# Kernel tuning notes

Measured on AMD Instinct MI355X. Metric: run time of the kernel, lower is better.

## Reference

```python
import jax, jax.numpy as jnp
import numpy as np

N_HEADS = 16
EPS = 1e-6  # WanSelfAttention passes eps=1e-6 to WanRMSNorm
ROPE_MAX = 1024


def _rmsnorm(v, g):
    # WanRMSNorm: normalize in fp32 over the full `dim`, then scale by weight
    v32 = v.astype(jnp.float32)
    n = v32 * jax.lax.rsqrt(jnp.mean(v32 * v32, axis=-1, keepdims=True) + EPS)
    return n * g


def _rope(x, f, h, w, fc, fs):
    # x: [b, s, n, d] with s == f*h*w. Complex rope: (a+bi) * (cos + i sin)
    b, s, n, d = x.shape
    c = d // 2
    c1 = c - 2 * (c // 3)
    c2 = c // 3

    def build(t):  # t: [ROPE_MAX, c] -> [1, s, 1, c]
        tf, th, tw = t[:, :c1], t[:, c1:c1 + c2], t[:, c1 + c2:]
        pf = jnp.broadcast_to(tf[:f, None, None, :], (f, h, w, c1))
        ph = jnp.broadcast_to(th[None, :h, None, :], (f, h, w, c2))
        pw = jnp.broadcast_to(tw[None, None, :w, :], (f, h, w, c2))
        return jnp.concatenate([pf, ph, pw], axis=-1).reshape(1, f * h * w, 1, c)

    cosv, sinv = build(fc), build(fs)
    xr = x.astype(jnp.float32).reshape(b, s, n, c, 2)
    a, bi = xr[..., 0], xr[..., 1]
    out_r = a * cosv - bi * sinv
    out_i = a * sinv + bi * cosv
    return jnp.stack([out_r, out_i], axis=-1).reshape(b, s, n, d)


def setup_inputs() -> dict:
    key = jax.random.key(0)
    ks = jax.random.split(key, 12)
    b, s, dim = 1, 2048, 2048
    n, d = N_HEADS, 2048 // N_HEADS  # d = 128, c = 64
    f, h, w = 2, 32, 32              # f*h*w == s
    c = d // 2
    c1 = c - 2 * (c // 3)
    c2 = c // 3

    # Realistic rope tables per band (cos/sin of pos * inv_freq)
    pos = np.arange(ROPE_MAX, dtype=np.float64)[:, None]
    ang = []
    for cx in (c1, c2, c2):
        inv = 1.0 / (10000.0 ** (np.arange(cx, dtype=np.float64) / cx))
        ang.append(pos * inv[None, :])
    ang = np.concatenate(ang, axis=1)
    freqs_cos = jnp.asarray(np.cos(ang), dtype=jnp.float32)
    freqs_sin = jnp.asarray(np.sin(ang), dtype=jnp.float32)

    scale = 1.0 / np.sqrt(dim)
    inp = {
        "x": jax.random.normal(ks[0], (b, s, dim), dtype=jnp.float32),
        "freqs_cos": freqs_cos,
        "freqs_sin": freqs_sin,
        "Wq": jax.random.normal(ks[1], (dim, dim), dtype=jnp.float32) * scale,
        "bq": jnp.zeros((dim,), dtype=jnp.float32),
        "Wk": jax.random.normal(ks[2], (dim, dim), dtype=jnp.float32) * scale,
        "bk": jnp.zeros((dim,), dtype=jnp.float32),
        "Wv": jax.random.normal(ks[3], (dim, dim), dtype=jnp.float32) * scale,
        "bv": jnp.zeros((dim,), dtype=jnp.float32),
        "Wo": jax.random.normal(ks[4], (dim, dim), dtype=jnp.float32) * scale,
        "bo": jnp.zeros((dim,), dtype=jnp.float32),
        "gq": jnp.ones((dim,), dtype=jnp.float32),
        "gk": jnp.ones((dim,), dtype=jnp.float32),
        "seq_lens": jnp.array([s], dtype=jnp.int32),
        "f": f,
        "h": h,
        "w": w,
    }
    return inp


def reference(x, freqs_cos, freqs_sin, Wq, bq, Wk, bk, Wv, bv, Wo, bo, gq, gk,
              seq_lens, f, h, w):
    b, s, dim = x.shape
    n = N_HEADS
    d = dim // n

    q = _rmsnorm(x @ Wq.T + bq, gq).reshape(b, s, n, d)
    k = _rmsnorm(x @ Wk.T + bk, gk).reshape(b, s, n, d)
    v = (x @ Wv.T + bv).reshape(b, s, n, d)

    q = _rope(q, f, h, w, freqs_cos, freqs_sin)
    k = _rope(k, f, h, w, freqs_cos, freqs_sin)

    scale = np.float32(1.0 / np.sqrt(d))
    scores = jnp.einsum('bqnd,bknd->bnqk', q, k) * scale  # [b,n,s,s]
    key_mask = jnp.arange(s)[None, :] < seq_lens[:, None]  # [b,s] (k_lens)
    scores = jnp.where(key_mask[:, None, None, :], scores, -jnp.inf)
    probs = jax.nn.softmax(scores, axis=-1)
    out = jnp.einsum('bnqk,bknd->bqnd', probs, v).reshape(b, s, dim)
    return out @ Wo.T + bo
```

## Files before the change

kernel.cpp:

```cpp
#include <hip/hip_runtime.h>
#include <cstdint>
#include <cmath>

typedef unsigned int uint;
typedef unsigned short ushort;
typedef __bf16 bf16_t;
typedef bf16_t bf16x8 __attribute__((ext_vector_type(8)));
typedef float f32x4 __attribute__((ext_vector_type(4)));
typedef float f32x16 __attribute__((ext_vector_type(16)));

#define LOG2E 1.44269504088896340736f

__device__ __forceinline__ ushort f2bf(float f) {
  uint x = __float_as_uint(f);
  x += 0x7fffu + ((x >> 16) & 1u);
  return (ushort)(x >> 16);
}
__device__ __forceinline__ uint pack2(float lo, float hi) {
  return (uint)f2bf(lo) | ((uint)f2bf(hi) << 16);
}
__device__ __forceinline__ uint cvt_pk_bf16(float lo, float hi) {
  uint r;
  asm("v_cvt_pk_bf16_f32 %0, %1, %2" : "=v"(r) : "v"(lo), "v"(hi));
  return r;
}

__device__ __forceinline__ void gload_lds16(const void* gsrc, void* ldsdst) {
  typedef const __attribute__((address_space(1))) unsigned int* gp_t;
  typedef __attribute__((address_space(3))) unsigned int* lp_t;
  __builtin_amdgcn_global_load_lds((gp_t)(uintptr_t)gsrc,
                                   (lp_t)(unsigned int)(uintptr_t)ldsdst,
                                   16, 0, 0);
}

__global__ __launch_bounds__(256) void cvt5(const float* __restrict__ x,
                                            const float* __restrict__ wq,
                                            const float* __restrict__ wk,
                                            const float* __restrict__ wv,
                                            const float* __restrict__ wo,
                                            ushort* __restrict__ xb,
                                            ushort* __restrict__ wqkv,
                                            ushort* __restrict__ wob,
                                            int nx8, int nw8) {
  const int y = blockIdx.y;
  const float* src;
  ushort* dst;
  int n8;
  if (y == 0)      { src = x;  dst = xb;  n8 = nx8; }
  else if (y == 4) { src = wo; dst = wob; n8 = nw8; }
  else {
    src = (y == 1) ? wq : (y == 2) ? wk : wv;
    dst = wqkv + (size_t)(y - 1) * nw8 * 8;
    n8 = nw8;
  }
  int i = blockIdx.x * blockDim.x + threadIdx.x;
  if (i >= n8) return;
  const float4* s4 = (const float4*)src;
  float4 a = s4[i * 2], b = s4[i * 2 + 1];
  uint4 o;
  o.x = pack2(a.x, a.y); o.y = pack2(a.z, a.w);
  o.z = pack2(b.x, b.y); o.w = pack2(b.z, b.w);
  ((uint4*)dst)[i] = o;
}

__global__ __launch_bounds__(512) void gemm_qkv192(const ushort* __restrict__ A,
                                                   const ushort* __restrict__ B,
                                                   const float* __restrict__ bq,
                                                   const float* __restrict__ bk,
                                                   const float* __restrict__ bv,
                                                   float* __restrict__ qpre,
                                                   float* __restrict__ kpre,
                                                   ushort* __restrict__ Vt,
                                                   int K, int S_) {
  __shared__ __align__(16) unsigned char ldsA[65536];
  __shared__ __align__(16) unsigned char ldsB[49152];
  const int t = threadIdx.x, l = t & 63;
  const int w = t >> 6;
  const int g = l >> 4, c = l & 15;
  const int wr = w >> 2, wc = w & 3;
  const int tm = blockIdx.y * 256, tn = blockIdx.x * 192;

  const int srow = t >> 3;
  const int schunk = (t & 7) ^ (srow & 7);
  const ushort* Ag = A + (size_t)(tm + srow) * K + schunk * 8;
  const ushort* Bg = B + (size_t)(tn + srow) * K + schunk * 8;
  const size_t rK64 = (size_t)64 * K;

#define STG_A(kt, u) gload_lds16(Ag + (size_t)(u) * rK64 + ((kt) << 6),   \
    ldsA + ((kt)&1) * 32768 + (u) * 8192 + t * 16)
#define STG_B(kt, u) gload_lds16(Bg + (size_t)(u) * rK64 + ((kt) << 6),   \
    ldsB + ((kt)&1) * 24576 + (u) * 8192 + t * 16)

  f32x4 acc[8][3] = {};
  bf16x8 af[2][2], bfr[3][2];
  const int cr = c * 128;
  const int sw0 = ((0 * 4 + g) ^ (c & 7)) << 4;
  const int sw1 = ((1 * 4 + g) ^ (c & 7)) << 4;

#define RDA(d, q) do {                                                               \
    _Pragma("unroll") for (int mm = 0; mm < 2; ++mm) {                               \
      const unsigned char* p_ = ldsA + (d)*32768 + (wr*128 + (q)*32 + mm*16)*128 + cr; \
      af[mm][0] = *(const bf16x8*)(p_ + sw0);                                        \
      af[mm][1] = *(const bf16x8*)(p_ + sw1); }                                      \
  } while (0)
#define RDB(d) do {                                                                 \
    _Pragma("unroll") for (int nn = 0; nn < 3; ++nn) {                              \
      const unsigned char* p_ = ldsB + (d)*24576 + (wc*48 + nn*16)*128 + cr;        \
      bfr[nn][0] = *(const bf16x8*)(p_ + sw0);                                      \
      bfr[nn][1] = *(const bf16x8*)(p_ + sw1); }                                    \
  } while (0)
#define MM(q) do {                                                                  \
    __builtin_amdgcn_s_setprio(1);                                                  \
    _Pragma("unroll") for (int mm = 0; mm < 2; ++mm)                                \
    _Pragma("unroll") for (int nn = 0; nn < 3; ++nn) {                              \
      acc[(q)*2+mm][nn] = __builtin_amdgcn_mfma_f32_16x16x32_bf16(                  \
          af[mm][0], bfr[nn][0], acc[(q)*2+mm][nn], 0, 0, 0);                       \
      acc[(q)*2+mm][nn] = __builtin_amdgcn_mfma_f32_16x16x32_bf16(                  \
          af[mm][1], bfr[nn][1], acc[(q)*2+mm][nn], 0, 0, 0); }                     \
    __builtin_amdgcn_s_setprio(0);                                                  \
  } while (0)
#define BAR() __builtin_amdgcn_s_barrier()

  STG_B(0, 0); STG_B(0, 1); STG_B(0, 2);
  STG_A(0, 0); STG_A(0, 1); STG_A(0, 2); STG_A(0, 3);
  STG_B(1, 0); STG_B(1, 1); STG_B(1, 2);
  STG_A(1, 0); STG_A(1, 1); STG_A(1, 2);
  asm volatile("s_waitcnt vmcnt(6)" ::: "memory");
  BAR();

  const int NITER = K >> 7;
  for (int i = 0; i < NITER; ++i) {
    const int k1 = 2 * i + 1, k2 = 2 * i + 2, k3 = 2 * i + 3;
    const bool st = (i + 1 < NITER);
    RDA(0, 0); RDB(0);
    STG_A(k1, 3);
    MM(0); BAR();
    RDA(0, 1);
    if (st) { STG_B(k2, 0); STG_B(k2, 1); }
    MM(1); BAR();
    RDA(0, 2);
    if (st) { STG_B(k2, 2); STG_A(k2, 0); }
    MM(2); BAR();
    RDA(0, 3);
    if (st) { STG_A(k2, 1); STG_A(k2, 2); }
    MM(3);
    if (st) asm volatile("s_waitcnt vmcnt(6)" ::: "memory");
    else    asm volatile("s_waitcnt vmcnt(0)" ::: "memory");
    BAR();
    RDA(1, 0); RDB(1);
    if (st) STG_A(k2, 3);
    MM(0); BAR();
    RDA(1, 1);
    if (st) { STG_B(k3, 0); STG_B(k3, 1); }
    MM(1); BAR();
    RDA(1, 2);
    if (st) { STG_B(k3, 2); STG_A(k3, 0); }
    MM(2); BAR();
    RDA(1, 3);
    if (st) { STG_A(k3, 1); STG_A(k3, 2); }
    MM(3);
    if (st) asm volatile("s_waitcnt vmcnt(6)" ::: "memory");
    else    asm volatile("s_waitcnt vmcnt(0)" ::: "memory");
    BAR();
  }

#undef STG_A
#undef STG_B
#undef RDA
#undef RDB
#undef MM
#undef BAR

#pragma unroll
  for (int n = 0; n < 3; ++n) {
    int col = tn + wc * 48 + n * 16 + c;
    int sel = col >> 11;
    if (sel < 2) {
      float* outp = sel ? kpre : qpre;
      const float* bias = sel ? bk : bq;
      int col2 = col & 2047;
      float bvv = bias[col2];
#pragma unroll
      for (int m = 0; m < 8; ++m) {
        int row0 = tm + wr * 128 + m * 16 + g * 4;
#pragma unroll
        for (int i = 0; i < 4; ++i)
          outp[(size_t)(row0 + i) * 2048 + col2] = acc[m][n][i] + bvv;
      }
    } else {
      int colv = col - 4096;
      float bvv = bv[colv];
#pragma unroll
      for (int m = 0; m < 8; ++m) {
        int row0 = tm + wr * 128 + m * 16 + g * 4;
        uint2 o;
        o.x = pack2(acc[m][n][0] + bvv, acc[m][n][1] + bvv);
        o.y = pack2(acc[m][n][2] + bvv, acc[m][n][3] + bvv);
        *(uint2*)(Vt + (size_t)colv * S_ + row0) = o;
      }
    }
  }
}

__global__ __launch_bounds__(512) void gemm_wo8p(const ushort* __restrict__ A,
                                                 const ushort* __restrict__ B,
                                                 const float* __restrict__ bo,
                                                 float* __restrict__ out, int K) {
  __shared__ __align__(16) unsigned char ldsA[32768];
  __shared__ __align__(16) unsigned char ldsB[32768];
  const int t = threadIdx.x, l = t & 63;
  const int w = t >> 6;
  const int g = l >> 4, c = l & 15;
  const int wr = w >> 2, wc = w & 3;
  const int tm = blockIdx.y * 128, tn = blockIdx.x * 128;

  const int srow = t >> 3;
  const int schunk = (t & 7) ^ (srow & 7);
  const ushort* Ag = A + (size_t)(tm + srow) * K + schunk * 8;
  const ushort* Bg = B + (size_t)(tn + srow) * K + schunk * 8;
  const size_t rK64 = (size_t)64 * K;

#define WSTG_A(kt, u) gload_lds16(Ag + (size_t)(u) * rK64 + ((kt) << 6),   \
    ldsA + ((kt)&1) * 16384 + (u) * 8192 + t * 16)
#define WSTG_B(kt, u) gload_lds16(Bg + (size_t)(u) * rK64 + ((kt) << 6),   \
    ldsB + ((kt)&1) * 16384 + (u) * 8192 + t * 16)

  f32x4 acc[4][2] = {};
  bf16x8 af[2][2], bfr[2][2];
  const int cr = c * 128;
  const int sw0 = ((0 * 4 + g) ^ (c & 7)) << 4;
  const int sw1 = ((1 * 4 + g) ^ (c & 7)) << 4;

#define WRDA(d, hf) do {                                                             \
    _Pragma("unroll") for (int mm = 0; mm < 2; ++mm) {                               \
      const unsigned char* p_ = ldsA + (d)*16384 + (wr*64 + ((hf)*2+mm)*16)*128 + cr; \
      af[mm][0] = *(const bf16x8*)(p_ + sw0);                                        \
      af[mm][1] = *(const bf16x8*)(p_ + sw1); }                                      \
  } while (0)
#define WRDB(d) do {                                                                \
    _Pragma("unroll") for (int nn = 0; nn < 2; ++nn) {                              \
      const unsigned char* p_ = ldsB + (d)*16384 + (wc*32 + nn*16)*128 + cr;        \
      bfr[nn][0] = *(const bf16x8*)(p_ + sw0);                                      \
      bfr[nn][1] = *(const bf16x8*)(p_ + sw1); }                                    \
  } while (0)
#define WMM(hf) do {                                                                \
    __builtin_amdgcn_s_setprio(1);                                                  \
    _Pragma("unroll") for (int mm = 0; mm < 2; ++mm)                                \
    _Pragma("unroll") for (int nn = 0; nn < 2; ++nn) {                              \
      acc[(hf)*2+mm][nn] = __builtin_amdgcn_mfma_f32_16x16x32_bf16(                 \
          af[mm][0], bfr[nn][0], acc[(hf)*2+mm][nn], 0, 0, 0);                      \
      acc[(hf)*2+mm][nn] = __builtin_amdgcn_mfma_f32_16x16x32_bf16(                 \
          af[mm][1], bfr[nn][1], acc[(hf)*2+mm][nn], 0, 0, 0); }                    \
    __builtin_amdgcn_s_setprio(0);                                                  \
  } while (0)
#define WBAR() __builtin_amdgcn_s_barrier()

  WSTG_B(0, 0); WSTG_B(0, 1); WSTG_A(0, 0); WSTG_A(0, 1);
  WSTG_B(1, 0); WSTG_B(1, 1);
  asm volatile("s_waitcnt vmcnt(2)" ::: "memory");
  WBAR();

  const int NITER = K >> 7;
  for (int i = 0; i < NITER; ++i) {
    const int k1 = 2 * i + 1, k2 = 2 * i + 2, k3 = 2 * i + 3;
    const bool st = (i + 1 < NITER);
    WRDA(0, 0); WRDB(0);
    WSTG_A(k1, 0); WSTG_A(k1, 1);
    WMM(0); WBAR();
    WRDA(0, 1);
    if (st) { WSTG_B(k2, 0); WSTG_B(k2, 1); }
    WMM(1);
    if (st) asm volatile("s_waitcnt vmcnt(2)" ::: "memory");
    else    asm volatile("s_waitcnt vmcnt(0)" ::: "memory");
    WBAR();
    WRDA(1, 0); WRDB(1);
    if (st) { WSTG_A(k2, 0); WSTG_A(k2, 1); }
    WMM(0); WBAR();
    WRDA(1, 1);
    if (st) { WSTG_B(k3, 0); WSTG_B(k3, 1); }
    WMM(1);
    if (st) asm volatile("s_waitcnt vmcnt(2)" ::: "memory");
    else    asm volatile("s_waitcnt vmcnt(0)" ::: "memory");
    WBAR();
  }

#undef WSTG_A
#undef WSTG_B
#undef WRDA
#undef WRDB
#undef WMM
#undef WBAR

#pragma unroll
  for (int n = 0; n < 2; ++n) {
    int col = tn + wc * 32 + n * 16 + c;
    float bvv = bo[col];
#pragma unroll
    for (int m = 0; m < 4; ++m) {
      int row0 = tm + wr * 64 + m * 16 + g * 4;
#pragma unroll
      for (int i = 0; i < 4; ++i)
        out[(size_t)(row0 + i) * 2048 + col] = acc[m][n][i] + bvv;
    }
  }
}

__global__ __launch_bounds__(256) void fuse_rms_rope(const float* __restrict__ qpre,
                                                     const float* __restrict__ kpre,
                                                     const float* __restrict__ gq,
                                                     const float* __restrict__ gk,
                                                     const float* __restrict__ fc,
                                                     const float* __restrict__ fs,
                                                     const int* __restrict__ pH,
                                                     const int* __restrict__ pW,
                                                     ushort* __restrict__ Qb,
                                                     ushort* __restrict__ Kb,
                                                     int dim, float foldq) {
  const int which = blockIdx.y;
  const float* pre = which ? kpre : qpre;
  const float* gw = which ? gk : gq;
  ushort* outp = which ? Kb : Qb;
  const float fold = which ? 1.0f : foldq;

  const int p = blockIdx.x, t = threadIdx.x;
  const float* row = pre + (size_t)p * dim;
  float v[8];
  {
    float4 a = *(const float4*)(row + t * 8);
    float4 b = *(const float4*)(row + t * 8 + 4);
    v[0] = a.x; v[1] = a.y; v[2] = a.z; v[3] = a.w;
    v[4] = b.x; v[5] = b.y; v[6] = b.z; v[7] = b.w;
  }
  float ss = 0.f;
#pragma unroll
  for (int i = 0; i < 8; ++i) ss += v[i] * v[i];
#pragma unroll
  for (int off = 32; off; off >>= 1) ss += __shfl_xor(ss, off);
  __shared__ float wsum[4];
  if ((t & 63) == 0) wsum[t >> 6] = ss;
  __syncthreads();
  float rstd = rsqrtf((wsum[0] + wsum[1] + wsum[2] + wsum[3]) * (1.0f / dim) + 1e-6f);
  float gv[8];
  {
    float4 a = *(const float4*)(gw + t * 8);
    float4 b = *(const float4*)(gw + t * 8 + 4);
    gv[0] = a.x; gv[1] = a.y; gv[2] = a.z; gv[3] = a.w;
    gv[4] = b.x; gv[5] = b.y; gv[6] = b.z; gv[7] = b.w;
  }
#pragma unroll
  for (int i = 0; i < 8; ++i) v[i] = v[i] * rstd * gv[i];

  const int H = pH[0], W = pW[0];
  const int hw = H * W;
  const int fr = p / hw;
  const int rem = p - fr * hw;
  const int hh = rem / W;
  const int ww = rem - hh * W;
  const int hd = dim / 16;
  const int cd = hd >> 1;
  const int c2 = cd / 3, c1 = cd - 2 * c2;
  const int j0 = ((t * 8) % hd) >> 1;

  uint ob[4];
#pragma unroll
  for (int q = 0; q < 4; ++q) {
    int j = j0 + q;
    int ri = (j < c1) ? fr : ((j < c1 + c2) ? hh : ww);
    float cs = fc[ri * cd + j];
    float sn = fs[ri * cd + j];
    float a = v[2 * q], b = v[2 * q + 1];
    ob[q] = pack2((a * cs - b * sn) * fold, (a * sn + b * cs) * fold);
  }
  uint4 o4; o4.x = ob[0]; o4.y = ob[1]; o4.z = ob[2]; o4.w = ob[3];
  *(uint4*)(outp + (size_t)p * dim + t * 8) = o4;
}

__global__ __launch_bounds__(512, 2) void attn32(const ushort* __restrict__ Qb,
                                                 const ushort* __restrict__ Kb,
                                                 const ushort* __restrict__ Vt,
                                                 ushort* __restrict__ Ob,
                                                 const int* __restrict__ seq_lens,
                                                 int S_, int DIMc) {
  __shared__ __align__(16) unsigned char smem[66560];
  float* mlbuf = (float*)(smem + 65536);
  const int t = threadIdx.x, l = t & 63, w = t >> 6;
  const int qsub = w & 3, ksp = w >> 2;
  const int h = l >> 5, ql = l & 31;

  const int orig = blockIdx.y * gridDim.x + blockIdx.x;
  const int nwg = gridDim.x * gridDim.y;
  const int lin = (orig & 7) * (nwg >> 3) + (orig >> 3);
  const int q0 = (lin % gridDim.x) * 128;
  const int head = lin / gridDim.x;
  const int kvlen = seq_lens[0];

  unsigned char* sk_s = smem + ksp * 16384;
  unsigned char* sv_s = smem + 32768 + ksp * 16384;

  bf16x8 qf[8];
  {
    const ushort* qp = Qb + (size_t)(q0 + qsub * 32 + ql) * DIMc + head * 128 + h * 8;
#pragma unroll
    for (int s = 0; s < 8; ++s) qf[s] = *(const bf16x8*)(qp + s * 16);
  }

  f32x16 ofr[4] = {};
  float m_run = -1e30f, l_run = 0.f;

  const int nt = (kvlen + 63) >> 6;
  const int half = (nt + 1) >> 1;
  const int tbase = ksp ? half : 0;
  const int mycnt = ksp ? (nt - half) : half;

#define MKK(IT, KO, KD) size_t KO; uint KD;                                     \
  { int kr_ = qsub * 16 + (IT) * 4 + (l >> 4); int kc_ = (l & 15) ^ (kr_ & 15); \
    KO = (size_t)kr_ * DIMc + head * 128 + kc_ * 8;                             \
    KD = (uint)(ksp * 16384 + qsub * 4096 + (IT) * 1024 + l * 16); }
#define MKV(IT, VO, VD) size_t VO; uint VD;                                     \
  { int vr_ = qsub * 32 + (IT) * 8 + (l >> 3); int vc_ = (l & 7) ^ (vr_ & 7);   \
    VO = (size_t)(head * 128 + vr_) * S_ + vc_ * 8;                             \
    VD = (uint)(32768 + ksp * 16384 + qsub * 4096 + (IT) * 1024 + l * 16); }
  MKK(0, kO0, kD0) MKK(1, kO1, kD1) MKK(2, kO2, kD2) MKK(3, kO3, kD3)
  MKV(0, vO0, vD0) MKV(1, vO1, vD1) MKV(2, vO2, vD2) MKV(3, vO3, vD3)
#undef MKK
#undef MKV

  uint4 rk0, rk1, rk2, rk3, rv0, rv1, rv2, rv3;
  if (mycnt > 0) {
    const size_t kbq = (size_t)(tbase * 64) * DIMc;
    const int vq = tbase * 64;
    rk0 = *(const uint4*)(Kb + kO0 + kbq);
    rk1 = *(const uint4*)(Kb + kO1 + kbq);
    rk2 = *(const uint4*)(Kb + kO2 + kbq);
    rk3 = *(const uint4*)(Kb + kO3 + kbq);
    rv0 = *(const uint4*)(Vt + vO0 + vq);
    rv1 = *(const uint4*)(Vt + vO1 + vq);
    rv2 = *(const uint4*)(Vt + vO2 + vq);
    rv3 = *(const uint4*)(Vt + vO3 + vq);
  }

  for (int tt = 0; tt < half; ++tt) {
    __builtin_amdgcn_s_barrier();
    if (tt < mycnt) {
      *(uint4*)(smem + kD0) = rk0; *(uint4*)(smem + kD1) = rk1;
      *(uint4*)(smem + kD2) = rk2; *(uint4*)(smem + kD3) = rk3;
      *(uint4*)(smem + vD0) = rv0; *(uint4*)(smem + vD1) = rv1;
      *(uint4*)(smem + vD2) = rv2; *(uint4*)(smem + vD3) = rv3;
      if (tt + 1 < mycnt) {
        const size_t kbq = (size_t)((tbase + tt + 1) * 64) * DIMc;
        const int vq = (tbase + tt + 1) * 64;
        rk0 = *(const uint4*)(Kb + kO0 + kbq);
        rk1 = *(const uint4*)(Kb + kO1 + kbq);
        rk2 = *(const uint4*)(Kb + kO2 + kbq);
        rk3 = *(const uint4*)(Kb + kO3 + kbq);
        rv0 = *(const uint4*)(Vt + vO0 + vq);
        rv1 = *(const uint4*)(Vt + vO1 + vq);
        rv2 = *(const uint4*)(Vt + vO2 + vq);
        rv3 = *(const uint4*)(Vt + vO3 + vq);
      }
    }
    asm volatile("s_waitcnt lgkmcnt(0)" ::: "memory");
    __builtin_amdgcn_s_barrier();
    __builtin_amdgcn_sched_barrier(0);
    if (tt >= mycnt) continue;
    const int kv0 = (tbase + tt) * 64;

    f32x16 sfr[2] = {};
    __builtin_amdgcn_s_setprio(1);
#pragma unroll
    for (int kb = 0; kb < 2; ++kb) {
      const unsigned char* kbp = sk_s + (kb * 32 + ql) * 256;
      const int rx = (kb * 32 + ql) & 15;
#pragma unroll
      for (int s = 0; s < 8; ++s) {
        bf16x8 kf = *(const bf16x8*)(kbp + (((s * 2 + h) ^ rx) << 4));
        sfr[kb] = __builtin_amdgcn_mfma_f32_32x32x16_bf16(kf, qf[s], sfr[kb], 0, 0, 0);
      }
    }
    __builtin_amdgcn_s_setprio(0);

    if (kv0 + 64 > kvlen) {
#pragma unroll
      for (int kb = 0; kb < 2; ++kb)
#pragma unroll
        for (int r = 0; r < 16; ++r) {
          int key = kv0 + kb * 32 + (r & 3) + 8 * (r >> 2) + 4 * h;
          if (key >= kvlen) sfr[kb][r] = -1e30f;
        }
    }

    float mt = -1e30f;
#pragma unroll
    for (int kb = 0; kb < 2; ++kb)
#pragma unroll
      for (int r = 0; r < 16; ++r) mt = fmaxf(mt, sfr[kb][r]);
    mt = fmaxf(mt, __shfl_xor(mt, 32));

    if (!__all(mt <= m_run + 8.0f)) {
      float m_new = fmaxf(m_run, mt);
      float fac = __builtin_amdgcn_exp2f(m_run - m_new);
      l_run *= fac;
#pragma unroll
      for (int df = 0; df < 4; ++df) ofr[df] *= fac;
      m_run = m_new;
    }

    float ls = 0.f;
    uint u[2][4][2];
#pragma unroll
    for (int kb = 0; kb < 2; ++kb)
#pragma unroll
      for (int G = 0; G < 4; ++G) {
        float p0 = __builtin_amdgcn_exp2f(sfr[kb][G * 4 + 0] - m_run);
        float p1 = __builtin_amdgcn_exp2f(sfr[kb][G * 4 + 1] - m_run);
        float p2 = __builtin_amdgcn_exp2f(sfr[kb][G * 4 + 2] - m_run);
        float p3 = __builtin_amdgcn_exp2f(sfr[kb][G * 4 + 3] - m_run);
        ls += (p0 + p1) + (p2 + p3);
        u[kb][G][0] = cvt_pk_bf16(p0, p1);
        u[kb][G][1] = cvt_pk_bf16(p2, p3);
      }
    ls += __shfl_xor(ls, 32);
    l_run += ls;

#pragma unroll
    for (int ks = 0; ks < 4; ++ks) {
      const int kb = ks >> 1, G0 = (ks & 1) * 2;
      uint own0 = h ? u[kb][G0 + 1][0] : u[kb][G0][0];
      uint own1 = h ? u[kb][G0 + 1][1] : u[kb][G0][1];
      uint snd0 = h ? u[kb][G0][0] : u[kb][G0 + 1][0];
      uint snd1 = h ? u[kb][G0][1] : u[kb][G0 + 1][1];
      uint rcv0 = __shfl_xor(snd0, 32);
      uint rcv1 = __shfl_xor(snd1, 32);
      union { uint4 q; bf16x8 b; } uu;
      uu.q.x = h ? rcv0 : own0;
      uu.q.y = h ? rcv1 : own1;
      uu.q.z = h ? own0 : rcv0;
      uu.q.w = h ? own1 : rcv1;
      __builtin_amdgcn_s_setprio(1);
#pragma unroll
      for (int df = 0; df < 4; ++df) {
        const int row = df * 32 + ql;
        bf16x8 vf = *(const bf16x8*)(sv_s + row * 128 + (((ks * 2 + h) ^ (row & 7)) << 4));
        ofr[df] = __builtin_amdgcn_mfma_f32_32x32x16_bf16(vf, uu.b, ofr[df], 0, 0, 0);
      }
      __builtin_amdgcn_s_setprio(0);
    }
  }

  __syncthreads();
  if (ksp == 1) {
    if (h == 0) { mlbuf[qsub * 64 + ql] = m_run; mlbuf[qsub * 64 + 32 + ql] = l_run; }
    float* ob = (float*)(smem + qsub * 16384);
#pragma unroll
    for (int df = 0; df < 4; ++df)
#pragma unroll
      for (int r = 0; r < 16; ++r) {
        int d = df * 32 + (r & 3) + 8 * (r >> 2) + 4 * h;
        ob[d * 32 + ql] = ofr[df][r];
      }
  }
  __syncthreads();
  if (ksp == 0) {
    float m2 = mlbuf[qsub * 64 + ql], l2 = mlbuf[qsub * 64 + 32 + ql];
    float mstar = fmaxf(m_run, m2);
    float f1 = __builtin_amdgcn_exp2f(m_run - mstar);
    float f2 = (l2 > 0.f) ? __builtin_amdgcn_exp2f(m2 - mstar) : 0.f;
    float lstar = l_run * f1 + l2 * f2;
    float inv = 1.0f / lstar;
    float a1 = f1 * inv, a2 = f2 * inv;
    const float* ob = (const float*)(smem + qsub * 16384);
    ushort* orow = Ob + (size_t)(q0 + qsub * 32 + ql) * DIMc + head * 128;
#pragma unroll
    for (int df = 0; df < 4; ++df)
#pragma unroll
      for (int G = 0; G < 4; ++G) {
        int d0 = df * 32 + 8 * G + 4 * h;
        float v0 = ofr[df][G * 4 + 0] * a1 + ob[(d0 + 0) * 32 + ql] * a2;
        float v1 = ofr[df][G * 4 + 1] * a1 + ob[(d0 + 1) * 32 + ql] * a2;
        float v2 = ofr[df][G * 4 + 2] * a1 + ob[(d0 + 2) * 32 + ql] * a2;
        float v3 = ofr[df][G * 4 + 3] * a1 + ob[(d0 + 3) * 32 + ql] * a2;
        uint2 o; o.x = pack2(v0, v1); o.y = pack2(v2, v3);
        *(uint2*)(orow + d0) = o;
      }
  }
}

extern "C" void kernel_launch(void* const* d_in, const int* in_sizes, int n_in,
                              void* d_out, int out_size, void* d_ws, size_t ws_size,
                              hipStream_t stream) {
  const float* x  = (const float*)d_in[0];
  const float* fc = (const float*)d_in[1];
  const float* fs = (const float*)d_in[2];
  const float* Wq = (const float*)d_in[3];
  const float* bq = (const float*)d_in[4];
  const float* Wk = (const float*)d_in[5];
  const float* bk = (const float*)d_in[6];
  const float* Wv = (const float*)d_in[7];
  const float* bv = (const float*)d_in[8];
  const float* Wo = (const float*)d_in[9];
  const float* bo = (const float*)d_in[10];
  const float* gq = (const float*)d_in[11];
  const float* gk = (const float*)d_in[12];
  const int* seq  = (const int*)d_in[13];
  const int* pH   = (const int*)d_in[15];
  const int* pW   = (const int*)d_in[16];

  const int DIMc = in_sizes[4];
  const int S_   = in_sizes[0] / DIMc;

  char* ws = (char*)d_ws;
  const size_t MB = 1024ull * 1024ull;
  ushort* xb    = (ushort*)(ws + 0 * MB);
  ushort* Wqkvb = (ushort*)(ws + 8 * MB);
  ushort* Wob   = (ushort*)(ws + 32 * MB);
  float*  qpre  = (float*)(ws + 40 * MB);
  float*  kpre  = (float*)(ws + 56 * MB);
  ushort* Qb    = (ushort*)(ws + 72 * MB);
  ushort* Kb    = (ushort*)(ws + 80 * MB);
  ushort* Vt    = (ushort*)(ws + 88 * MB);
  ushort* Ob    = (ushort*)(ws + 40 * MB);

  const int nx8 = (S_ * DIMc) / 8;
  const int nw8 = (DIMc * DIMc) / 8;
  const int nmax = (nx8 > nw8 ? nx8 : nw8);
  cvt5<<<dim3((nmax + 255) / 256, 5), 256, 0, stream>>>(x, Wq, Wk, Wv, Wo,
                                                        xb, Wqkvb, Wob, nx8, nw8);

  gemm_qkv192<<<dim3(3 * DIMc / 192, S_ / 256), 512, 0, stream>>>(
      xb, Wqkvb, bq, bk, bv, qpre, kpre, Vt, DIMc, S_);

  const float foldq = LOG2E / sqrtf((float)(DIMc / 16));
  fuse_rms_rope<<<dim3(S_, 2), 256, 0, stream>>>(qpre, kpre, gq, gk, fc, fs, pH, pW,
                                                 Qb, Kb, DIMc, foldq);

  attn32<<<dim3(S_ / 128, 16), 512, 0, stream>>>(Qb, Kb, Vt, Ob, seq, S_, DIMc);

  gemm_wo8p<<<dim3(DIMc / 128, S_ / 128), 512, 0, stream>>>(Ob, Wob, bo,
                                                            (float*)d_out, DIMc);
}
```

Before: 155.1 us.

## Double-buffer K/V tiles in LDS to drop one barrier per iteration

After: 155.7 us. About the same (+0.4%).

```diff
diff --git a/kernel.cpp b/kernel.cpp
--- a/kernel.cpp
+++ b/kernel.cpp
@@ -381,8 +381,8 @@
                                                  ushort* __restrict__ Ob,
                                                  const int* __restrict__ seq_lens,
                                                  int S_, int DIMc) {
-  __shared__ __align__(16) unsigned char smem[66560];
-  float* mlbuf = (float*)(smem + 65536);
+  __shared__ __align__(16) unsigned char smem[134144];
+  float* mlbuf = (float*)(smem + 133120);
   const int t = threadIdx.x, l = t & 63, w = t >> 6;
   const int qsub = w & 3, ksp = w >> 2;
   const int h = l >> 5, ql = l & 31;
@@ -393,9 +393,6 @@
   const int q0 = (lin % gridDim.x) * 128;
   const int head = lin / gridDim.x;
   const int kvlen = seq_lens[0];
-
-  unsigned char* sk_s = smem + ksp * 16384;
-  unsigned char* sv_s = smem + 32768 + ksp * 16384;
 
   bf16x8 qf[8];
   {
@@ -425,127 +422,131 @@
 #undef MKK
 #undef MKV
 
+#define LOAD_TILE(TIX) do {                                                     \
+    const size_t kbq_ = (size_t)((TIX) * 64) * DIMc;                            \
+    const int vq_ = (TIX) * 64;                                                 \
+    rk0 = *(const uint4*)(Kb + kO0 + kbq_);                                     \
+    rk1 = *(const uint4*)(Kb + kO1 + kbq_);                                     \
+    rk2 = *(const uint4*)(Kb + kO2 + kbq_);                                     \
+    rk3 = *(const uint4*)(Kb + kO3 + kbq_);                                     \
+    rv0 = *(const uint4*)(Vt + vO0 + vq_);                                      \
+    rv1 = *(const uint4*)(Vt + vO1 + vq_);                                      \
+    rv2 = *(const uint4*)(Vt + vO2 + vq_);                                      \
+    rv3 = *(const uint4*)(Vt + vO3 + vq_);                                      \
+  } while (0)
+#define WRITE_TILE(BOFF) do {                                                   \
+    *(uint4*)(smem + (BOFF) + kD0) = rk0; *(uint4*)(smem + (BOFF) + kD1) = rk1; \
+    *(uint4*)(smem + (BOFF) + kD2) = rk2; *(uint4*)(smem + (BOFF) + kD3) = rk3; \
+    *(uint4*)(smem + (BOFF) + vD0) = rv0; *(uint4*)(smem + (BOFF) + vD1) = rv1; \
+    *(uint4*)(smem + (BOFF) + vD2) = rv2; *(uint4*)(smem + (BOFF) + vD3) = rv3; \
+  } while (0)
+
   uint4 rk0, rk1, rk2, rk3, rv0, rv1, rv2, rv3;
-  if (mycnt > 0) {
-    const size_t kbq = (size_t)(tbase * 64) * DIMc;
-    const int vq = tbase * 64;
-    rk0 = *(const uint4*)(Kb + kO0 + kbq);
-    rk1 = *(const uint4*)(Kb + kO1 + kbq);
-    rk2 = *(const uint4*)(Kb + kO2 + kbq);
-    rk3 = *(const uint4*)(Kb + kO3 + kbq);
-    rv0 = *(const uint4*)(Vt + vO0 + vq);
-    rv1 = *(const uint4*)(Vt + vO1 + vq);
-    rv2 = *(const uint4*)(Vt + vO2 + vq);
-    rv3 = *(const uint4*)(Vt + vO3 + vq);
-  }
+  if (mycnt > 0) { LOAD_TILE(tbase); WRITE_TILE(0u); }
+  if (mycnt > 1) LOAD_TILE(tbase + 1);
+  asm volatile("s_waitcnt lgkmcnt(0)" ::: "memory");
+  __builtin_amdgcn_s_barrier();
+  __builtin_amdgcn_sched_barrier(0);
 
   for (int tt = 0; tt < half; ++tt) {
-    __builtin_amdgcn_s_barrier();
+    const uint cb = (uint)(tt & 1) * 66560u;
+    const uint wb = (uint)((tt + 1) & 1) * 66560u;
+    asm volatile("s_waitcnt vmcnt(0)" ::: "memory");
+    if (tt + 1 < mycnt) WRITE_TILE(wb);
+    if (tt + 2 < mycnt) LOAD_TILE(tbase + tt + 2);
     if (tt < mycnt) {
-      *(uint4*)(smem + kD0) = rk0; *(uint4*)(smem + kD1) = rk1;
-      *(uint4*)(smem + kD2) = rk2; *(uint4*)(smem + kD3) = rk3;
-      *(uint4*)(smem + vD0) = rv0; *(uint4*)(smem + vD1) = rv1;
-      *(uint4*)(smem + vD2) = rv2; *(uint4*)(smem + vD3) = rv3;
-      if (tt + 1 < mycnt) {
-        const size_t kbq = (size_t)((tbase + tt + 1) * 64) * DIMc;
-        const int vq = (tbase + tt + 1) * 64;
-        rk0 = *(const uint4*)(Kb + kO0 + kbq);
-        rk1 = *(const uint4*)(Kb + kO1 + kbq);
-        rk2 = *(const uint4*)(Kb + kO2 + kbq);
-        rk3 = *(const uint4*)(Kb + kO3 + kbq);
-        rv0 = *(const uint4*)(Vt + vO0 + vq);
-        rv1 = *(const uint4*)(Vt + vO1 + vq);
-        rv2 = *(const uint4*)(Vt + vO2 + vq);
-        rv3 = *(const uint4*)(Vt + vO3 + vq);
+      const unsigned char* sk_s = smem + cb + ksp * 16384;
+      const unsigned char* sv_s = smem + cb + 32768 + ksp * 16384;
+      const int kv0 = (tbase + tt) * 64;
+
+      f32x16 sfr[2] = {};
+      __builtin_amdgcn_s_setprio(1);
+#pragma unroll
+      for (int kb = 0; kb < 2; ++kb) {
+        const unsigned char* kbp = sk_s + (kb * 32 + ql) * 256;
+        const int rx = (kb * 32 + ql) & 15;
+#pragma unroll
+        for (int s = 0; s < 8; ++s) {
+          bf16x8 kf = *(const bf16x8*)(kbp + (((s * 2 + h) ^ rx) << 4));
+          sfr[kb] = __builtin_amdgcn_mfma_f32_32x32x16_bf16(kf, qf[s], sfr[kb], 0, 0, 0);
+        }
+      }
+      __builtin_amdgcn_s_setprio(0);
+
+      if (kv0 + 64 > kvlen) {
+#pragma unroll
+        for (int kb = 0; kb < 2; ++kb)
+#pragma unroll
+          for (int r = 0; r < 16; ++r) {
+            int key = kv0 + kb * 32 + (r & 3) + 8 * (r >> 2) + 4 * h;
+            if (key >= kvlen) sfr[kb][r] = -1e30f;
+          }
+      }
+
+      float mt = -1e30f;
+#pragma unroll
+      for (int kb = 0; kb < 2; ++kb)
+#pragma unroll
+        for (int r = 0; r < 16; ++r) mt = fmaxf(mt, sfr[kb][r]);
+      mt = fmaxf(mt, __shfl_xor(mt, 32));
+
+      if (!__all(mt <= m_run + 8.0f)) {
+        float m_new = fmaxf(m_run, mt);
+        float fac = __builtin_amdgcn_exp2f(m_run - m_new);
+        l_run *= fac;
+#pragma unroll
+        for (int df = 0; df < 4; ++df) ofr[df] *= fac;
+        m_run = m_new;
+      }
+
+      float ls = 0.f;
+      uint u[2][4][2];
+#pragma unroll
+      for (int kb = 0; kb < 2; ++kb)
+#pragma unroll
+        for (int G = 0; G < 4; ++G) {
+          float p0 = __builtin_amdgcn_exp2f(sfr[kb][G * 4 + 0] - m_run);
+          float p1 = __builtin_amdgcn_exp2f(sfr[kb][G * 4 + 1] - m_run);
+          float p2 = __builtin_amdgcn_exp2f(sfr[kb][G * 4 + 2] - m_run);
+          float p3 = __builtin_amdgcn_exp2f(sfr[kb][G * 4 + 3] - m_run);
+          ls += (p0 + p1) + (p2 + p3);
+          u[kb][G][0] = cvt_pk_bf16(p0, p1);
+          u[kb][G][1] = cvt_pk_bf16(p2, p3);
+        }
+      ls += __shfl_xor(ls, 32);
+      l_run += ls;
+
+#pragma unroll
+      for (int ks = 0; ks < 4; ++ks) {
+        const int kb = ks >> 1, G0 = (ks & 1) * 2;
+        uint own0 = h ? u[kb][G0 + 1][0] : u[kb][G0][0];
+        uint own1 = h ? u[kb][G0 + 1][1] : u[kb][G0][1];
+        uint snd0 = h ? u[kb][G0][0] : u[kb][G0 + 1][0];
+        uint snd1 = h ? u[kb][G0][1] : u[kb][G0 + 1][1];
+        uint rcv0 = __shfl_xor(snd0, 32);
+        uint rcv1 = __shfl_xor(snd1, 32);
+        union { uint4 q; bf16x8 b; } uu;
+        uu.q.x = h ? rcv0 : own0;
+        uu.q.y = h ? rcv1 : own1;
+        uu.q.z = h ? own0 : rcv0;
+        uu.q.w = h ? own1 : rcv1;
+        __builtin_amdgcn_s_setprio(1);
+#pragma unroll
+        for (int df = 0; df < 4; ++df) {
+          const int row = df * 32 + ql;
+          bf16x8 vf = *(const bf16x8*)(sv_s + row * 128 + (((ks * 2 + h) ^ (row & 7)) << 4));
+          ofr[df] = __builtin_amdgcn_mfma_f32_32x32x16_bf16(vf, uu.b, ofr[df], 0, 0, 0);
+        }
+        __builtin_amdgcn_s_setprio(0);
       }
     }
     asm volatile("s_waitcnt lgkmcnt(0)" ::: "memory");
     __builtin_amdgcn_s_barrier();
     __builtin_amdgcn_sched_barrier(0);
-    if (tt >= mycnt) continue;
-    const int kv0 = (tbase + tt) * 64;
-
-    f32x16 sfr[2] = {};
-    __builtin_amdgcn_s_setprio(1);
-#pragma unroll
-    for (int kb = 0; kb < 2; ++kb) {
-      const unsigned char* kbp = sk_s + (kb * 32 + ql) * 256;
-      const int rx = (kb * 32 + ql) & 15;
-#pragma unroll
-      for (int s = 0; s < 8; ++s) {
-        bf16x8 kf = *(const bf16x8*)(kbp + (((s * 2 + h) ^ rx) << 4));
-        sfr[kb] = __builtin_amdgcn_mfma_f32_32x32x16_bf16(kf, qf[s], sfr[kb], 0, 0, 0);
-      }
-    }
-    __builtin_amdgcn_s_setprio(0);
-
-    if (kv0 + 64 > kvlen) {
-#pragma unroll
-      for (int kb = 0; kb < 2; ++kb)
-#pragma unroll
-        for (int r = 0; r < 16; ++r) {
-          int key = kv0 + kb * 32 + (r & 3) + 8 * (r >> 2) + 4 * h;
-          if (key >= kvlen) sfr[kb][r] = -1e30f;
-        }
-    }
-
-    float mt = -1e30f;
-#pragma unroll
-    for (int kb = 0; kb < 2; ++kb)
-#pragma unroll
-      for (int r = 0; r < 16; ++r) mt = fmaxf(mt, sfr[kb][r]);
-    mt = fmaxf(mt, __shfl_xor(mt, 32));
-
-    if (!__all(mt <= m_run + 8.0f)) {
-      float m_new = fmaxf(m_run, mt);
-      float fac = __builtin_amdgcn_exp2f(m_run - m_new);
-      l_run *= fac;
-#pragma unroll
-      for (int df = 0; df < 4; ++df) ofr[df] *= fac;
-      m_run = m_new;
-    }
-
-    float ls = 0.f;
-    uint u[2][4][2];
-#pragma unroll
-    for (int kb = 0; kb < 2; ++kb)
-#pragma unroll
-      for (int G = 0; G < 4; ++G) {
-        float p0 = __builtin_amdgcn_exp2f(sfr[kb][G * 4 + 0] - m_run);
-        float p1 = __builtin_amdgcn_exp2f(sfr[kb][G * 4 + 1] - m_run);
-        float p2 = __builtin_amdgcn_exp2f(sfr[kb][G * 4 + 2] - m_run);
-        float p3 = __builtin_amdgcn_exp2f(sfr[kb][G * 4 + 3] - m_run);
-        ls += (p0 + p1) + (p2 + p3);
-        u[kb][G][0] = cvt_pk_bf16(p0, p1);
-        u[kb][G][1] = cvt_pk_bf16(p2, p3);
-      }
-    ls += __shfl_xor(ls, 32);
-    l_run += ls;
-
-#pragma unroll
-    for (int ks = 0; ks < 4; ++ks) {
-      const int kb = ks >> 1, G0 = (ks & 1) * 2;
-      uint own0 = h ? u[kb][G0 + 1][0] : u[kb][G0][0];
-      uint own1 = h ? u[kb][G0 + 1][1] : u[kb][G0][1];
-      uint snd0 = h ? u[kb][G0][0] : u[kb][G0 + 1][0];
-      uint snd1 = h ? u[kb][G0][1] : u[kb][G0 + 1][1];
-      uint rcv0 = __shfl_xor(snd0, 32);
-      uint rcv1 = __shfl_xor(snd1, 32);
-      union { uint4 q; bf16x8 b; } uu;
-      uu.q.x = h ? rcv0 : own0;
-      uu.q.y = h ? rcv1 : own1;
-      uu.q.z = h ? own0 : rcv0;
-      uu.q.w = h ? own1 : rcv1;
-      __builtin_amdgcn_s_setprio(1);
-#pragma unroll
-      for (int df = 0; df < 4; ++df) {
-        const int row = df * 32 + ql;
-        bf16x8 vf = *(const bf16x8*)(sv_s + row * 128 + (((ks * 2 + h) ^ (row & 7)) << 4));
-        ofr[df] = __builtin_amdgcn_mfma_f32_32x32x16_bf16(vf, uu.b, ofr[df], 0, 0, 0);
-      }
-      __builtin_amdgcn_s_setprio(0);
-    }
-  }
+  }
+
+#undef LOAD_TILE
+#undef WRITE_TILE
 
   __syncthreads();
   if (ksp == 1) {
```

## Split attention KV range across two grid slices and merge partials

Applied to the files above, without the earlier changes.

Measured after the change: 411.1 us. +165.1%, slower.

```diff
diff --git a/kernel.cpp b/kernel.cpp
--- a/kernel.cpp
+++ b/kernel.cpp
@@ -375,10 +375,11 @@
   *(uint4*)(outp + (size_t)p * dim + t * 8) = o4;
 }
 
-__global__ __launch_bounds__(512, 2) void attn32(const ushort* __restrict__ Qb,
+__global__ __launch_bounds__(512, 4) void attn32(const ushort* __restrict__ Qb,
                                                  const ushort* __restrict__ Kb,
                                                  const ushort* __restrict__ Vt,
-                                                 ushort* __restrict__ Ob,
+                                                 float* __restrict__ pO,
+                                                 float* __restrict__ pml,
                                                  const int* __restrict__ seq_lens,
                                                  int S_, int DIMc) {
   __shared__ __align__(16) unsigned char smem[66560];
@@ -386,6 +387,7 @@
   const int t = threadIdx.x, l = t & 63, w = t >> 6;
   const int qsub = w & 3, ksp = w >> 2;
   const int h = l >> 5, ql = l & 31;
+  const int z = blockIdx.z;
 
   const int orig = blockIdx.y * gridDim.x + blockIdx.x;
   const int nwg = gridDim.x * gridDim.y;
@@ -408,9 +410,12 @@
   float m_run = -1e30f, l_run = 0.f;
 
   const int nt = (kvlen + 63) >> 6;
-  const int half = (nt + 1) >> 1;
-  const int tbase = ksp ? half : 0;
-  const int mycnt = ksp ? (nt - half) : half;
+  const int ntz0 = (nt + 1) >> 1;
+  const int zbase = z ? ntz0 : 0;
+  const int ntz = z ? (nt - ntz0) : ntz0;
+  const int half = (ntz + 1) >> 1;
+  const int tbase = zbase + (ksp ? half : 0);
+  const int mycnt = ksp ? (ntz - half) : ((ntz < half) ? ntz : half);
 
 #define MKK(IT, KO, KD) size_t KO; uint KD;                                     \
   { int kr_ = qsub * 16 + (IT) * 4 + (l >> 4); int kc_ = (l & 15) ^ (kr_ & 15); \
@@ -561,28 +566,55 @@
   }
   __syncthreads();
   if (ksp == 0) {
+    const int row = q0 + qsub * 32 + ql;
     float m2 = mlbuf[qsub * 64 + ql], l2 = mlbuf[qsub * 64 + 32 + ql];
     float mstar = fmaxf(m_run, m2);
     float f1 = __builtin_amdgcn_exp2f(m_run - mstar);
     float f2 = (l2 > 0.f) ? __builtin_amdgcn_exp2f(m2 - mstar) : 0.f;
     float lstar = l_run * f1 + l2 * f2;
-    float inv = 1.0f / lstar;
-    float a1 = f1 * inv, a2 = f2 * inv;
+    if (h == 0) {
+      size_t mi = ((size_t)z * 2048 + row) * 32 + head * 2;
+      pml[mi] = mstar;
+      pml[mi + 1] = lstar;
+    }
     const float* ob = (const float*)(smem + qsub * 16384);
-    ushort* orow = Ob + (size_t)(q0 + qsub * 32 + ql) * DIMc + head * 128;
+    float* prow = pO + (size_t)z * 4194304 + (size_t)row * 2048 + head * 128;
 #pragma unroll
     for (int df = 0; df < 4; ++df)
 #pragma unroll
       for (int G = 0; G < 4; ++G) {
         int d0 = df * 32 + 8 * G + 4 * h;
-        float v0 = ofr[df][G * 4 + 0] * a1 + ob[(d0 + 0) * 32 + ql] * a2;
-        float v1 = ofr[df][G * 4 + 1] * a1 + ob[(d0 + 1) * 32 + ql] * a2;
-        float v2 = ofr[df][G * 4 + 2] * a1 + ob[(d0 + 2) * 32 + ql] * a2;
-        float v3 = ofr[df][G * 4 + 3] * a1 + ob[(d0 + 3) * 32 + ql] * a2;
-        uint2 o; o.x = pack2(v0, v1); o.y = pack2(v2, v3);
-        *(uint2*)(orow + d0) = o;
-      }
-  }
+        float4 o;
+        o.x = ofr[df][G * 4 + 0] * f1 + ob[(d0 + 0) * 32 + ql] * f2;
+        o.y = ofr[df][G * 4 + 1] * f1 + ob[(d0 + 1) * 32 + ql] * f2;
+        o.z = ofr[df][G * 4 + 2] * f1 + ob[(d0 + 2) * 32 + ql] * f2;
+        o.w = ofr[df][G * 4 + 3] * f1 + ob[(d0 + 3) * 32 + ql] * f2;
+        *(float4*)(prow + d0) = o;
+      }
+  }
+}
+
+__global__ __launch_bounds__(256) void attn_merge(const float* __restrict__ pO,
+                                                  const float* __restrict__ pml,
+                                                  ushort* __restrict__ Ob, int n4) {
+  int i = blockIdx.x * 256 + threadIdx.x;
+  if (i >= n4) return;
+  int row = i >> 9;
+  int head = (i & 511) >> 5;
+  size_t mi = (size_t)row * 32 + head * 2;
+  float m1 = pml[mi], l1 = pml[mi + 1];
+  float m2 = pml[65536 + mi], l2 = pml[65536 + mi + 1];
+  float M = fmaxf(m1, m2);
+  float e1 = __builtin_amdgcn_exp2f(m1 - M);
+  float e2 = __builtin_amdgcn_exp2f(m2 - M);
+  float inv = 1.0f / (l1 * e1 + l2 * e2);
+  e1 *= inv; e2 *= inv;
+  float4 o1 = ((const float4*)pO)[i];
+  float4 o2 = ((const float4*)pO)[i + 1048576];
+  uint2 o;
+  o.x = pack2(o1.x * e1 + o2.x * e2, o1.y * e1 + o2.y * e2);
+  o.y = pack2(o1.z * e1 + o2.z * e2, o1.w * e1 + o2.w * e2);
+  ((uint2*)Ob)[i] = o;
 }
 
 extern "C" void kernel_launch(void* const* d_in, const int* in_sizes, int n_in,
@@ -618,7 +650,9 @@
   ushort* Qb    = (ushort*)(ws + 72 * MB);
   ushort* Kb    = (ushort*)(ws + 80 * MB);
   ushort* Vt    = (ushort*)(ws + 88 * MB);
-  ushort* Ob    = (ushort*)(ws + 40 * MB);
+  float*  pO    = (float*)(ws + 40 * MB);
+  float*  pml   = (float*)(ws + 8 * MB);
+  ushort* Ob    = (ushort*)(ws + 0 * MB);
 
   const int nx8 = (S_ * DIMc) / 8;
   const int nw8 = (DIMc * DIMc) / 8;
@@ -633,7 +667,9 @@
   fuse_rms_rope<<<dim3(S_, 2), 256, 0, stream>>>(qpre, kpre, gq, gk, fc, fs, pH, pW,
                                                  Qb, Kb, DIMc, foldq);
 
-  attn32<<<dim3(S_ / 128, 16), 512, 0, stream>>>(Qb, Kb, Vt, Ob, seq, S_, DIMc);
+  attn32<<<dim3(S_ / 128, 16, 2), 512, 0, stream>>>(Qb, Kb, Vt, pO, pml, seq, S_, DIMc);
+  attn_merge<<<(S_ * DIMc / 4 + 255) / 256, 256, 0, stream>>>(pO, pml, Ob,
+                                                              S_ * DIMc / 4);
 
   gemm_wo8p<<<dim3(DIMc / 128, S_ / 128), 512, 0, stream>>>(Ob, Wob, bo,
                                                             (float*)d_out, DIMc);
```
